# Kernel tuning notes

Hardware: AMD Instinct MI355X
Metric: run time of the kernel (lower is better)

The kernel has to match this reference:

```python
import jax, jax.numpy as jnp
import numpy as np

N, E, IN, H, G = 100000, 1600000, 64, 108, 128
N_LAYERS = 2  # hidden_dims=[108,108] -> 1 layer from hidden_dims[1:] + 1 final layer


def setup_inputs() -> dict:
    key = jax.random.key(0)
    ks = jax.random.split(key, 13)
    s = lambda fan_in: 1.0 / np.sqrt(fan_in)
    inp = {
        "nodes_feat": jax.random.normal(ks[0], (N, IN), jnp.float32),
        "edges_feat": jax.random.normal(ks[1], (E, 1), jnp.float32),
        "nodes_num_norm_sqrt": jax.random.uniform(ks[2], (N,), jnp.float32),
        "edges_num_norm_sqrt": jax.random.uniform(ks[3], (E,), jnp.float32),
        "W_emb": jax.random.uniform(ks[4], (IN, H), jnp.float32, -s(IN), s(IN)),
        "b_emb": jax.random.uniform(ks[5], (H,), jnp.float32, -s(IN), s(IN)),
        "pool_W": jax.random.uniform(ks[6], (N_LAYERS, H, H), jnp.float32, -s(H), s(H)),
        "pool_b": jax.random.uniform(ks[7], (N_LAYERS, H), jnp.float32, -s(H), s(H)),
        "app_W": jax.random.uniform(ks[8], (N_LAYERS, 2 * H, H), jnp.float32, -s(2 * H), s(2 * H)),
        "app_b": jax.random.uniform(ks[9], (N_LAYERS, H), jnp.float32, -s(2 * H), s(2 * H)),
        "src": jax.random.randint(ks[10], (E,), 0, N, jnp.int64 if jax.config.jax_enable_x64 else jnp.int32),
        "dst": jax.random.randint(ks[11], (E,), 0, N, jnp.int64 if jax.config.jax_enable_x64 else jnp.int32),
        "graph_ids": jnp.sort(jax.random.randint(ks[12], (N,), 0, G, jnp.int64 if jax.config.jax_enable_x64 else jnp.int32)),
        "n_graphs": G,
    }
    return inp


def reference(nodes_feat, edges_feat, nodes_num_norm_sqrt, edges_num_norm_sqrt,
              W_emb, b_emb, pool_W, pool_b, app_W, app_b,
              src, dst, graph_ids, n_graphs):
    n = nodes_feat.shape[0]
    # embedding_h
    h = nodes_feat @ W_emb + b_emb  # [N, H]
    # in-degree for mean aggregation (dropout = 0.0 so omitted)
    deg = jax.ops.segment_sum(jnp.ones((src.shape[0],), h.dtype), dst, num_segments=n)
    deg = jnp.maximum(deg, 1.0)[:, None]  # [N, 1]
    for i in range(pool_W.shape[0]):
        h_in = h
        # meanpool aggregator: per-message linear+ReLU == per-node transform then gather
        z = jax.nn.relu(h @ pool_W[i] + pool_b[i])  # [N, H]
        c = jax.ops.segment_sum(z[src], dst, num_segments=n) / deg  # mean over neighbors
        # NodeApply: linear(concat(h, c)) -> L2 normalize -> activation
        b = jnp.concatenate([h, c], axis=1) @ app_W[i] + app_b[i]
        b = b / jnp.maximum(jnp.linalg.norm(b, axis=1, keepdims=True), 1e-12)
        h = h_in + jax.nn.relu(b)  # residual (dims match: 108 == 108)
    # dgl.mean_nodes readout per graph
    cnt = jax.ops.segment_sum(jnp.ones((n,), h.dtype), graph_ids, num_segments=n_graphs)
    hg = jax.ops.segment_sum(h, graph_ids, num_segments=n_graphs) / jnp.maximum(cnt, 1.0)[:, None]
    return hg  # [n_graphs, H]
```

## Files before the change

kernel.cpp:

```cpp
#include <hip/hip_runtime.h>

#define HDIM 108
constexpr int G_GRAPHS = 128;
constexpr int MAXNB = 1024;
constexpr int CAP = 2560;

typedef _Float16 half8 __attribute__((ext_vector_type(8)));
typedef _Float16 half4v __attribute__((ext_vector_type(4)));
typedef float floatx4 __attribute__((ext_vector_type(4)));
typedef float floatx2 __attribute__((ext_vector_type(2)));

__device__ inline unsigned char f32_to_fp8(float t) {
#if __has_builtin(__builtin_amdgcn_cvt_pk_fp8_f32)
  return (unsigned char)(__builtin_amdgcn_cvt_pk_fp8_f32(t, t, 0, false) & 0xFF);
#else
  t = fminf(t, 448.f);
  if (t < 0.015625f) return (unsigned char)__float2int_rn(t * 512.f);
  unsigned u = __float_as_uint(t);
  unsigned lsb = (u >> 20) & 1;
  u += 0x7FFFFu + lsb;
  int e = (int)((u >> 23) & 0xFF) - 127;
  if (e > 8) return 0x7E;
  return (unsigned char)(((e + 7) << 3) | ((u >> 20) & 7));
#endif
}

template <bool HI>
__device__ inline floatx2 fp8x2_to_f32(unsigned v) {
#if __has_builtin(__builtin_amdgcn_cvt_pk_f32_fp8)
  return __builtin_amdgcn_cvt_pk_f32_fp8((int)v, HI);
#else
  unsigned b0 = HI ? ((v >> 16) & 0xFF) : (v & 0xFF);
  unsigned b1 = HI ? ((v >> 24) & 0xFF) : ((v >> 8) & 0xFF);
  floatx2 r;
  {
    unsigned s = b0 >> 7, e = (b0 >> 3) & 0xF, m = b0 & 7;
    float f = (e == 0) ? (float)m * 0.001953125f
                       : __uint_as_float(((e + 120u) << 23) | (m << 20));
    r[0] = s ? -f : f;
  }
  {
    unsigned s = b1 >> 7, e = (b1 >> 3) & 0xF, m = b1 & 7;
    float f = (e == 0) ? (float)m * 0.001953125f
                       : __uint_as_float(((e + 120u) << 23) | (m << 20));
    r[1] = s ? -f : f;
  }
  return r;
#endif
}

__global__ __launch_bounds__(1024) void k_scatter(const int* __restrict__ src, const int* __restrict__ dst,
                                                  int* __restrict__ gcur, int* __restrict__ ebuf,
                                                  const float* __restrict__ W_emb,
                                                  const float* __restrict__ pool_W,
                                                  const float* __restrict__ app_W,
                                                  _Float16* __restrict__ wte,
                                                  _Float16* __restrict__ wtp,
                                                  _Float16* __restrict__ wta,
                                                  int E, int nb) {
  __shared__ int hist[MAXNB];
  const int tid = threadIdx.x;
  const int e0 = blockIdx.x * 16384;

  int gi = blockIdx.x * 1024 + tid;
  if (gi < 86016) {
    const float* srcw;
    _Float16* dstw;
    int Kpad, K, split, rel;
    if (gi < 7168)       { rel = gi;          srcw = W_emb;          dstw = wte;         Kpad = 64;  K = 64;  split = 0; }
    else if (gi < 21504) { rel = gi - 7168;   srcw = pool_W;         dstw = wtp;         Kpad = 128; K = 108; split = 0; }
    else if (gi < 35840) { rel = gi - 21504;  srcw = pool_W + 11664; dstw = wtp + 14336; Kpad = 128; K = 108; split = 0; }
    else if (gi < 60928) { rel = gi - 35840;  srcw = app_W;          dstw = wta;         Kpad = 224; K = 216; split = 1; }
    else                 { rel = gi - 60928;  srcw = app_W + 23328;  dstw = wta + 25088; Kpad = 224; K = 216; split = 1; }
    int n = rel / Kpad, k = rel - n * Kpad;
    int ks;
    if (split) ks = (k < 108) ? k : (k >= 112 && k < 220) ? (k - 4) : -1;
    else       ks = (k < K) ? k : -1;
    float v = (n < 108 && ks >= 0) ? srcw[ks * 108 + n] : 0.f;
    dstw[rel] = (_Float16)v;
  }

  for (int b = tid; b < nb; b += 1024) hist[b] = 0;
  __syncthreads();
#pragma unroll
  for (int it = 0; it < 16; it++) {
    int e = e0 + it * 1024 + tid;
    if (e < E) atomicAdd(&hist[dst[e] >> 7], 1);
  }
  __syncthreads();
  for (int b = tid; b < nb; b += 1024) {
    int h = hist[b];
    hist[b] = h ? atomicAdd(&gcur[b * 16], h) : 0;
  }
  __syncthreads();
#pragma unroll
  for (int it = 0; it < 16; it++) {
    int e = e0 + it * 1024 + tid;
    if (e < E) {
      int d = dst[e];
      int b = d >> 7;
      int rank = atomicAdd(&hist[b], 1);
      if (rank < CAP) ebuf[(size_t)b * CAP + rank] = src[e] | ((d & 127) << 20);
    }
  }
}

__global__ __launch_bounds__(1024) void k_bagg(const unsigned char* __restrict__ z, const int* __restrict__ ebuf,
                                               const int* __restrict__ gcur, _Float16* __restrict__ c16,
                                               int N, int nb) {
  __shared__ int cnts[128];
  __shared__ int scanb[128];
  __shared__ int off[129];
  __shared__ int ecur[128];
  __shared__ int esrc[CAP];
  const int tid = threadIdx.x;
  const int b = blockIdx.x;
  const int v0 = b << 7;
  int cntb = gcur[b * 16];
  if (cntb > CAP) cntb = CAP;
  const int* eb = ebuf + (size_t)b * CAP;

  if (tid < 128) cnts[tid] = 0;
  __syncthreads();
  for (int i = tid; i < cntb; i += 1024) atomicAdd(&cnts[eb[i] >> 20], 1);
  __syncthreads();
  if (tid < 128) scanb[tid] = cnts[tid];
  __syncthreads();
#pragma unroll
  for (int st = 1; st < 128; st <<= 1) {
    int v = 0;
    if (tid < 128 && tid >= st) v = scanb[tid - st];
    __syncthreads();
    if (tid < 128) scanb[tid] += v;
    __syncthreads();
  }
  if (tid == 0) off[0] = 0;
  if (tid < 128) {
    off[tid + 1] = scanb[tid];
    ecur[tid] = scanb[tid] - cnts[tid];
  }
  __syncthreads();
  for (int i = tid; i < cntb; i += 1024) {
    int e = eb[i];
    int p = atomicAdd(&ecur[e >> 20], 1);
    esrc[p] = e & 0xFFFFF;
  }
  __syncthreads();

  const int lane = tid & 31;
  const int grp = tid >> 5;
  if (lane >= 28) return;
  const unsigned char* __restrict__ zl = z + lane * 4;
#pragma unroll 1
  for (int r = grp; r < 128; r += 32) {
    int v = v0 + r;
    if (v >= N) continue;
    int s = off[r], e2 = off[r + 1];
    float a0 = 0.f, a1 = 0.f, a2 = 0.f, a3 = 0.f;
    int j = s;
    for (; j + 4 <= e2; j += 4) {
      unsigned q0 = *(const unsigned*)(zl + (size_t)esrc[j] * 128);
      unsigned q1 = *(const unsigned*)(zl + (size_t)esrc[j + 1] * 128);
      unsigned q2 = *(const unsigned*)(zl + (size_t)esrc[j + 2] * 128);
      unsigned q3 = *(const unsigned*)(zl + (size_t)esrc[j + 3] * 128);
      floatx2 l0 = fp8x2_to_f32<false>(q0), h0 = fp8x2_to_f32<true>(q0);
      floatx2 l1 = fp8x2_to_f32<false>(q1), h1 = fp8x2_to_f32<true>(q1);
      floatx2 l2 = fp8x2_to_f32<false>(q2), h2 = fp8x2_to_f32<true>(q2);
      floatx2 l3 = fp8x2_to_f32<false>(q3), h3 = fp8x2_to_f32<true>(q3);
      a0 += (l0[0] + l1[0]) + (l2[0] + l3[0]);
      a1 += (l0[1] + l1[1]) + (l2[1] + l3[1]);
      a2 += (h0[0] + h1[0]) + (h2[0] + h3[0]);
      a3 += (h0[1] + h1[1]) + (h2[1] + h3[1]);
    }
    for (; j < e2; j++) {
      unsigned q0 = *(const unsigned*)(zl + (size_t)esrc[j] * 128);
      floatx2 l0 = fp8x2_to_f32<false>(q0), h0 = fp8x2_to_f32<true>(q0);
      a0 += l0[0]; a1 += l0[1]; a2 += h0[0]; a3 += h0[1];
    }
    int d = e2 - s;
    float inv = 1.f / (float)(d > 0 ? d : 1);
    half4v r4;
    r4[0] = (_Float16)(a0 * inv); r4[1] = (_Float16)(a1 * inv);
    r4[2] = (_Float16)(a2 * inv); r4[3] = (_Float16)(a3 * inv);
    *(half4v*)(c16 + (size_t)v * 112 + lane * 4) = r4;
  }
}

template <int KCH, int MODE>
__global__ __launch_bounds__(256) void k_mmf(const void* Asrc, const _Float16* __restrict__ c16,
                                             const _Float16* __restrict__ Wt, const float* __restrict__ bias,
                                             void* outp, int N) {
  constexpr int KW = KCH * 32;
  __shared__ _Float16 As[64 * 40];
  __shared__ _Float16 Ws[112 * 40];

  const int tid = threadIdx.x;
  const int wave = tid >> 6;
  const int lane = tid & 63;
  const int lo = lane & 15;
  const int quad = lane >> 4;
  const int n0 = blockIdx.x * 64;
  const _Float16* h16 = (const _Float16*)Asrc;
  const float* feat = (const float*)Asrc;

  floatx4 acc[7];
#pragma unroll
  for (int ct = 0; ct < 7; ct++) {
    floatx4 zz = {0.f, 0.f, 0.f, 0.f};
    acc[ct] = zz;
  }

#pragma unroll 1
  for (int kc = 0; kc < KCH; kc++) {
    {
      int r = tid >> 2, sg = tid & 3;
      int gn = n0 + r;
      int k = kc * 32 + sg * 8;
      half8 v = {0, 0, 0, 0, 0, 0, 0, 0};
      if (gn < N) {
        if (MODE == 0) {
          float4 f0 = *(const float4*)(feat + (size_t)gn * 64 + k);
          float4 f1 = *(const float4*)(feat + (size_t)gn * 64 + k + 4);
          v[0] = (_Float16)f0.x; v[1] = (_Float16)f0.y; v[2] = (_Float16)f0.z; v[3] = (_Float16)f0.w;
          v[4] = (_Float16)f1.x; v[5] = (_Float16)f1.y; v[6] = (_Float16)f1.z; v[7] = (_Float16)f1.w;
        } else if (MODE == 2) {
          const _Float16* sp = (k < 112) ? (h16 + (size_t)gn * 112 + k)
                                         : (c16 + (size_t)gn * 112 + (k - 112));
          v = *(const half8*)sp;
        } else {
          if (k < 112) v = *(const half8*)(h16 + (size_t)gn * 112 + k);
        }
      }
      *(half8*)&As[r * 40 + sg * 8] = v;
    }
#pragma unroll
    for (int it = 0; it < 2; it++) {
      int idx = tid + it * 256;
      if (idx < 448) {
        int nrow = idx >> 2, sg = idx & 3;
        half8 v = *(const half8*)(Wt + (size_t)nrow * KW + kc * 32 + sg * 8);
        *(half8*)&Ws[nrow * 40 + sg * 8] = v;
      }
    }
    __syncthreads();

    half8 a = *(const half8*)&As[(wave * 16 + lo) * 40 + quad * 8];
#pragma unroll
    for (int ct = 0; ct < 7; ct++) {
      half8 b = *(const half8*)&Ws[(ct * 16 + lo) * 40 + quad * 8];
      acc[ct] = __builtin_amdgcn_mfma_f32_16x16x32_f16(a, b, acc[ct], 0, 0, 0);
    }
    __syncthreads();
  }

  float bias_v[7];
#pragma unroll
  for (int ct = 0; ct < 7; ct++) {
    int col = ct * 16 + lo;
    bias_v[ct] = (col < 108) ? bias[col] : 0.f;
  }

  if (MODE == 2) {
    _Float16* out16 = (_Float16*)outp;
#pragma unroll
    for (int reg = 0; reg < 4; reg++) {
      int gr = n0 + wave * 16 + quad * 4 + reg;
      float bv[7];
      float ssq = 0.f;
#pragma unroll
      for (int ct = 0; ct < 7; ct++) {
        float t = acc[ct][reg] + bias_v[ct];
        bv[ct] = t;
        ssq += t * t;
      }
#pragma unroll
      for (int s = 1; s < 16; s <<= 1) ssq += __shfl_xor(ssq, s, 16);
      float scale = 1.f / fmaxf(sqrtf(ssq), 1e-12f);
      if (gr < N) {
        _Float16* hp = out16 + (size_t)gr * 112 + lo;
#pragma unroll
        for (int ct = 0; ct < 7; ct++) {
          float hv = (float)hp[ct * 16];
          hp[ct * 16] = (_Float16)(hv + fmaxf(bv[ct] * scale, 0.f));
        }
      }
    }
  } else if (MODE == 1) {
    unsigned char* outb = (unsigned char*)outp;
#pragma unroll
    for (int reg = 0; reg < 4; reg++) {
      int gr = n0 + wave * 16 + quad * 4 + reg;
      if (gr < N) {
        unsigned char* op = outb + (size_t)gr * 128 + lo;
#pragma unroll
        for (int ct = 0; ct < 7; ct++) {
          float t = fmaxf(acc[ct][reg] + bias_v[ct], 0.f);
          op[ct * 16] = f32_to_fp8(t);
        }
      }
    }
  } else {
    _Float16* out16 = (_Float16*)outp;
#pragma unroll
    for (int reg = 0; reg < 4; reg++) {
      int gr = n0 + wave * 16 + quad * 4 + reg;
      if (gr < N) {
        _Float16* op = out16 + (size_t)gr * 112 + lo;
#pragma unroll
        for (int ct = 0; ct < 7; ct++) {
          float t = acc[ct][reg] + bias_v[ct];
          op[ct * 16] = (_Float16)t;
        }
      }
    }
  }
}

__global__ __launch_bounds__(256) void k_readout(const _Float16* __restrict__ h, const int* __restrict__ gid,
                                                 float* __restrict__ hg, int N) {
  const int CH = 64;
  const int lane = threadIdx.x & 31;
  const int grp = threadIdx.x >> 5;
  int start = (blockIdx.x * 8 + grp) * CH;
  if (start >= N || lane >= 27) return;
  int end = min(start + CH, N);
  float a0 = 0.f, a1 = 0.f, a2 = 0.f, a3 = 0.f;
  int cur = gid[start];
  for (int i = start; i < end; i++) {
    int g = gid[i];
    if (g != cur) {
      float* base = &hg[(size_t)cur * HDIM + lane * 4];
      atomicAdd(base + 0, a0); atomicAdd(base + 1, a1);
      atomicAdd(base + 2, a2); atomicAdd(base + 3, a3);
      a0 = a1 = a2 = a3 = 0.f;
      cur = g;
    }
    half4v v = *(const half4v*)(h + (size_t)i * 112 + lane * 4);
    a0 += (float)v[0]; a1 += (float)v[1]; a2 += (float)v[2]; a3 += (float)v[3];
  }
  float* base = &hg[(size_t)cur * HDIM + lane * 4];
  atomicAdd(base + 0, a0); atomicAdd(base + 1, a1);
  atomicAdd(base + 2, a2); atomicAdd(base + 3, a3);
}

__global__ __launch_bounds__(256) void k_div(const float* __restrict__ hg, const int* __restrict__ gid,
                                             float* __restrict__ out, int total, int N) {
  int i = blockIdx.x * 256 + threadIdx.x;
  if (i < total) {
    int g = i / HDIM;
    int lo = 0, hi = N;
    while (lo < hi) { int m = (lo + hi) >> 1; if (gid[m] < g) lo = m + 1; else hi = m; }
    int lb = lo;
    lo = 0; hi = N;
    while (lo < hi) { int m = (lo + hi) >> 1; if (gid[m] <= g) lo = m + 1; else hi = m; }
    int c = lo - lb;
    out[i] = hg[i] / (float)(c > 0 ? c : 1);
  }
}

extern "C" void kernel_launch(void* const* d_in, const int* in_sizes, int n_in,
                              void* d_out, int out_size, void* d_ws, size_t ws_size,
                              hipStream_t stream) {
  (void)n_in; (void)ws_size; (void)out_size;
  const float* nodes_feat = (const float*)d_in[0];
  const float* W_emb = (const float*)d_in[4];
  const float* b_emb = (const float*)d_in[5];
  const float* pool_W = (const float*)d_in[6];
  const float* pool_b = (const float*)d_in[7];
  const float* app_W = (const float*)d_in[8];
  const float* app_b = (const float*)d_in[9];
  const int* src = (const int*)d_in[10];
  const int* dst = (const int*)d_in[11];
  const int* gid = (const int*)d_in[12];
  const int N = in_sizes[2];
  const int E = in_sizes[10];
  float* out = (float*)d_out;

  const int nb = (N + 127) >> 7;

  char* ws = (char*)d_ws;
  size_t off = 0;
  auto alloc = [&](size_t bytes) -> size_t {
    size_t o = off;
    off += (bytes + 1023) & ~size_t(1023);
    return o;
  };
  size_t o_gcur = alloc((size_t)MAXNB * 16 * 4);
  size_t o_hg   = alloc((size_t)G_GRAPHS * HDIM * 4);
  size_t zero_bytes = off;
  size_t o_ebuf = alloc((size_t)MAXNB * CAP * 4);
  size_t o_h  = alloc((size_t)N * 112 * 2);
  size_t o_z  = alloc((size_t)N * 128);
  size_t o_c  = alloc((size_t)N * 112 * 2);
  size_t o_we = alloc((size_t)112 * 64 * 2);
  size_t o_wp = alloc((size_t)2 * 112 * 128 * 2);
  size_t o_wa = alloc((size_t)2 * 112 * 224 * 2);

  int*           gcur = (int*)(ws + o_gcur);
  float*         hg   = (float*)(ws + o_hg);
  int*           ebuf = (int*)(ws + o_ebuf);
  _Float16*      h16  = (_Float16*)(ws + o_h);
  unsigned char* z8   = (unsigned char*)(ws + o_z);
  _Float16*      c16  = (_Float16*)(ws + o_c);
  _Float16*      wte  = (_Float16*)(ws + o_we);
  _Float16*      wtp  = (_Float16*)(ws + o_wp);
  _Float16*      wta  = (_Float16*)(ws + o_wa);

  (void)hipMemsetAsync(d_ws, 0, zero_bytes, stream);

  k_scatter<<<(E + 16383) / 16384, 1024, 0, stream>>>(src, dst, gcur, ebuf,
                                                      W_emb, pool_W, app_W,
                                                      wte, wtp, wta, E, nb);

  const int nbMM = (N + 63) / 64;
  k_mmf<2, 0><<<nbMM, 256, 0, stream>>>(nodes_feat, nullptr, wte, b_emb, h16, N);

  for (int i = 0; i < 2; i++) {
    k_mmf<4, 1><<<nbMM, 256, 0, stream>>>(h16, nullptr, wtp + i * 14336,
                                          pool_b + i * HDIM, z8, N);
    k_bagg<<<nb, 1024, 0, stream>>>(z8, ebuf, gcur, c16, N, nb);
    k_mmf<7, 2><<<nbMM, 256, 0, stream>>>(h16, c16, wta + i * 25088,
                                          app_b + i * HDIM, h16, N);
  }

  k_readout<<<(N + 8 * 64 - 1) / (8 * 64), 256, 0, stream>>>(h16, gid, hg, N);
  k_div<<<(G_GRAPHS * HDIM + 255) / 256, 256, 0, stream>>>(hg, gid, out, G_GRAPHS * HDIM, N);
}
```

Before: 337.3 us.

## Split aggregation blocks in half, stage full A tile once, shrink readout chunks

The aggregation kernel now launches two 512-thread blocks per 128-node bucket, each handling 64 destination nodes. Each block still scans the whole bucket's edge list and skips edges for the other half. In the matmul kernel, the entire A row-tile for all K is staged into LDS in one pass. Weight fragments are read straight from global memory (relying on cache) instead of going through LDS, which removes the per-K-chunk barriers. The readout chunk size drops from 64 to 16 nodes, giving more parallel groups at the cost of more atomics.

```diff
diff --git a/kernel.cpp b/kernel.cpp
--- a/kernel.cpp
+++ b/kernel.cpp
@@ -4,6 +4,7 @@
 constexpr int G_GRAPHS = 128;
 constexpr int MAXNB = 1024;
 constexpr int CAP = 2560;
+constexpr int ESCAP = 1536;
 
 typedef _Float16 half8 __attribute__((ext_vector_type(8)));
 typedef _Float16 half4v __attribute__((ext_vector_type(4)));
@@ -105,45 +106,52 @@
   }
 }
 
-__global__ __launch_bounds__(1024) void k_bagg(const unsigned char* __restrict__ z, const int* __restrict__ ebuf,
-                                               const int* __restrict__ gcur, _Float16* __restrict__ c16,
-                                               int N, int nb) {
-  __shared__ int cnts[128];
-  __shared__ int scanb[128];
-  __shared__ int off[129];
-  __shared__ int ecur[128];
-  __shared__ int esrc[CAP];
+__global__ __launch_bounds__(512) void k_bagg(const unsigned char* __restrict__ z, const int* __restrict__ ebuf,
+                                              const int* __restrict__ gcur, _Float16* __restrict__ c16,
+                                              int N, int nb) {
+  __shared__ int cnts[64];
+  __shared__ int scanb[64];
+  __shared__ int off[65];
+  __shared__ int ecur[64];
+  __shared__ int esrc[ESCAP];
   const int tid = threadIdx.x;
-  const int b = blockIdx.x;
-  const int v0 = b << 7;
+  const int b = blockIdx.x >> 1;
+  const int half = blockIdx.x & 1;
+  const int v0 = (b << 7) + (half << 6);
   int cntb = gcur[b * 16];
   if (cntb > CAP) cntb = CAP;
   const int* eb = ebuf + (size_t)b * CAP;
 
-  if (tid < 128) cnts[tid] = 0;
-  __syncthreads();
-  for (int i = tid; i < cntb; i += 1024) atomicAdd(&cnts[eb[i] >> 20], 1);
-  __syncthreads();
-  if (tid < 128) scanb[tid] = cnts[tid];
-  __syncthreads();
-#pragma unroll
-  for (int st = 1; st < 128; st <<= 1) {
+  if (tid < 64) cnts[tid] = 0;
+  __syncthreads();
+  for (int i = tid; i < cntb; i += 512) {
+    int ld = eb[i] >> 20;
+    if ((ld >> 6) == half) atomicAdd(&cnts[ld & 63], 1);
+  }
+  __syncthreads();
+  if (tid < 64) scanb[tid] = cnts[tid];
+  __syncthreads();
+#pragma unroll
+  for (int st = 1; st < 64; st <<= 1) {
     int v = 0;
-    if (tid < 128 && tid >= st) v = scanb[tid - st];
+    if (tid < 64 && tid >= st) v = scanb[tid - st];
     __syncthreads();
-    if (tid < 128) scanb[tid] += v;
+    if (tid < 64) scanb[tid] += v;
     __syncthreads();
   }
   if (tid == 0) off[0] = 0;
-  if (tid < 128) {
+  if (tid < 64) {
     off[tid + 1] = scanb[tid];
     ecur[tid] = scanb[tid] - cnts[tid];
   }
   __syncthreads();
-  for (int i = tid; i < cntb; i += 1024) {
+  for (int i = tid; i < cntb; i += 512) {
     int e = eb[i];
-    int p = atomicAdd(&ecur[e >> 20], 1);
-    esrc[p] = e & 0xFFFFF;
+    int ld = e >> 20;
+    if ((ld >> 6) == half) {
+      int p = atomicAdd(&ecur[ld & 63], 1);
+      if (p < ESCAP) esrc[p] = e & 0xFFFFF;
+    }
   }
   __syncthreads();
 
@@ -152,10 +160,12 @@
   if (lane >= 28) return;
   const unsigned char* __restrict__ zl = z + lane * 4;
 #pragma unroll 1
-  for (int r = grp; r < 128; r += 32) {
+  for (int r = grp; r < 64; r += 16) {
     int v = v0 + r;
     if (v >= N) continue;
     int s = off[r], e2 = off[r + 1];
+    if (e2 > ESCAP) e2 = ESCAP;
+    if (s > ESCAP) s = ESCAP;
     float a0 = 0.f, a1 = 0.f, a2 = 0.f, a3 = 0.f;
     int j = s;
     for (; j + 4 <= e2; j += 4) {
@@ -191,8 +201,9 @@
                                              const _Float16* __restrict__ Wt, const float* __restrict__ bias,
                                              void* outp, int N) {
   constexpr int KW = KCH * 32;
-  __shared__ _Float16 As[64 * 40];
-  __shared__ _Float16 Ws[112 * 40];
+  constexpr int AST = KW + 8;
+  constexpr int SEGS = KW / 8;
+  __shared__ _Float16 As[64 * AST];
 
   const int tid = threadIdx.x;
   const int wave = tid >> 6;
@@ -203,19 +214,13 @@
   const _Float16* h16 = (const _Float16*)Asrc;
   const float* feat = (const float*)Asrc;
 
-  floatx4 acc[7];
-#pragma unroll
-  for (int ct = 0; ct < 7; ct++) {
-    floatx4 zz = {0.f, 0.f, 0.f, 0.f};
-    acc[ct] = zz;
-  }
-
-#pragma unroll 1
-  for (int kc = 0; kc < KCH; kc++) {
-    {
-      int r = tid >> 2, sg = tid & 3;
+#pragma unroll
+  for (int it = 0; it < (64 * SEGS + 255) / 256; it++) {
+    int idx = tid + it * 256;
+    if (idx < 64 * SEGS) {
+      int r = idx / SEGS, sg = idx - r * SEGS;
       int gn = n0 + r;
-      int k = kc * 32 + sg * 8;
+      int k = sg * 8;
       half8 v = {0, 0, 0, 0, 0, 0, 0, 0};
       if (gn < N) {
         if (MODE == 0) {
@@ -231,26 +236,26 @@
           if (k < 112) v = *(const half8*)(h16 + (size_t)gn * 112 + k);
         }
       }
-      *(half8*)&As[r * 40 + sg * 8] = v;
-    }
-#pragma unroll
-    for (int it = 0; it < 2; it++) {
-      int idx = tid + it * 256;
-      if (idx < 448) {
-        int nrow = idx >> 2, sg = idx & 3;
-        half8 v = *(const half8*)(Wt + (size_t)nrow * KW + kc * 32 + sg * 8);
-        *(half8*)&Ws[nrow * 40 + sg * 8] = v;
-      }
-    }
-    __syncthreads();
-
-    half8 a = *(const half8*)&As[(wave * 16 + lo) * 40 + quad * 8];
+      *(half8*)&As[r * AST + sg * 8] = v;
+    }
+  }
+  __syncthreads();
+
+  floatx4 acc[7];
+#pragma unroll
+  for (int ct = 0; ct < 7; ct++) {
+    floatx4 zz = {0.f, 0.f, 0.f, 0.f};
+    acc[ct] = zz;
+  }
+
+#pragma unroll
+  for (int kc = 0; kc < KCH; kc++) {
+    half8 a = *(const half8*)&As[(wave * 16 + lo) * AST + kc * 32 + quad * 8];
 #pragma unroll
     for (int ct = 0; ct < 7; ct++) {
-      half8 b = *(const half8*)&Ws[(ct * 16 + lo) * 40 + quad * 8];
+      half8 b = *(const half8*)(Wt + (size_t)(ct * 16 + lo) * KW + kc * 32 + quad * 8);
       acc[ct] = __builtin_amdgcn_mfma_f32_16x16x32_f16(a, b, acc[ct], 0, 0, 0);
     }
-    __syncthreads();
   }
 
   float bias_v[7];
@@ -318,7 +323,7 @@
 
 __global__ __launch_bounds__(256) void k_readout(const _Float16* __restrict__ h, const int* __restrict__ gid,
                                                  float* __restrict__ hg, int N) {
-  const int CH = 64;
+  const int CH = 16;
   const int lane = threadIdx.x & 31;
   const int grp = threadIdx.x >> 5;
   int start = (blockIdx.x * 8 + grp) * CH;
@@ -418,11 +423,11 @@
   for (int i = 0; i < 2; i++) {
     k_mmf<4, 1><<<nbMM, 256, 0, stream>>>(h16, nullptr, wtp + i * 14336,
                                           pool_b + i * HDIM, z8, N);
-    k_bagg<<<nb, 1024, 0, stream>>>(z8, ebuf, gcur, c16, N, nb);
+    k_bagg<<<nb * 2, 512, 0, stream>>>(z8, ebuf, gcur, c16, N, nb);
     k_mmf<7, 2><<<nbMM, 256, 0, stream>>>(h16, c16, wta + i * 25088,
                                           app_b + i * HDIM, h16, N);
   }
 
-  k_readout<<<(N + 8 * 64 - 1) / (8 * 64), 256, 0, stream>>>(h16, gid, hg, N);
+  k_readout<<<(N + 8 * 16 - 1) / (8 * 16), 256, 0, stream>>>(h16, gid, hg, N);
   k_div<<<(G_GRAPHS * HDIM + 255) / 256, 256, 0, stream>>>(hg, gid, out, G_GRAPHS * HDIM, N);
 }
```

Result: slower. 396.1 us (+17.4%).
